# Kernel tuning notes

Measured on AMD Instinct MI355X. Metric: run time of the kernel, lower is better.

The kernel has to match this reference:

```python
import jax, jax.numpy as jnp
import numpy as np

N_FEATURES = 256
TOPK = 32
WINDOW = 128
EMBED = 128
BATCH = 64
ALPHA = 0.2  # LeakyReLU negative slope


def setup_inputs() -> dict:
    key = jax.random.key(0)
    ks = jax.random.split(key, 8)
    x_n = jax.random.normal(ks[0], (BATCH, N_FEATURES, WINDOW), jnp.float32)
    x_e = jax.random.normal(ks[1], (N_FEATURES, TOPK), jnp.float32)
    edge_indices = jax.random.randint(ks[2], (2, N_FEATURES * TOPK), 0, N_FEATURES, dtype=jnp.int32)
    all_embeddings = jax.random.normal(ks[3], (N_FEATURES, EMBED), jnp.float32)
    # lin_n: Linear(window_size, embed_dim)
    W_n = jax.random.normal(ks[4], (WINDOW, EMBED), jnp.float32) * (1.0 / np.sqrt(WINDOW))
    b_n = jax.random.normal(ks[5], (EMBED,), jnp.float32) * 0.01
    # attention vector a: [2*embed_dim, 1], xavier-like scale
    a = jax.random.normal(ks[6], (2 * EMBED, 1), jnp.float32) * (1.414 / np.sqrt(2 * EMBED))
    bias_n = jax.random.normal(ks[7], (N_FEATURES, TOPK), jnp.float32) * 0.02
    return {"x_n": x_n, "x_e": x_e, "edge_indices": edge_indices,
            "all_embeddings": all_embeddings, "W_n": W_n, "b_n": b_n,
            "a": a, "bias_n": bias_n}


def reference(x_n, x_e, edge_indices, all_embeddings, W_n, b_n, a, bias_n):
    B, NF, _ = x_n.shape
    K, E = TOPK, EMBED
    lrelu = lambda t: jax.nn.leaky_relu(t, negative_slope=ALPHA)

    # Wx_n = lin_n(x_n): [B, NF, E]
    Wx_n = jnp.einsum('bnw,we->bne', x_n, W_n) + b_n

    nbr = edge_indices[0].reshape(NF, K)  # neighbor ids per node

    # _make_node_attention_input (faithful, including the cat-then-view mixing):
    # repeat_interleave(K, dim=1) -> [B, NF, K, E]
    rep = jnp.broadcast_to(Wx_n[:, :, None, :], (B, NF, K, E))
    alt = Wx_n[:, nbr]  # gather: [B, NF, K, E]
    # cat on dim=2 -> [B, NF, 2K, E]; view -> [B, NF, K, 2E]
    a_input_n = jnp.concatenate([rep, alt], axis=2).reshape(B, NF, K, 2 * E)

    # e_n = leakyrelu(a_input_n @ a).squeeze(3): [B, NF, K]
    e_n = lrelu(jnp.einsum('bnkd,d->bnk', a_input_n, a[:, 0]))
    e_n = e_n + jnp.nan_to_num(bias_n)

    # softmax over topk neighbors; dropout is a no-op in eval mode
    attention_n = jax.nn.softmax(e_n, axis=2)

    # weighted aggregate of gathered neighbor features
    h_n = lrelu(attention_n[..., None] * alt)  # [B, NF, K, E]
    return h_n
```

## Files before the change

kernel.cpp:

```cpp
#include <hip/hip_runtime.h>

#define NFEAT 256
#define TK    32
#define WIN   128
#define EMB   128
#define NBATCH 64
#define ALPHA 0.2f
#define MROWS (NBATCH * NFEAT)

__device__ __forceinline__ float lrelu(float x) { return x > 0.f ? x : ALPHA * x; }

__global__ __launch_bounds__(256) void gemm_wx(
    const float* __restrict__ x,
    const float* __restrict__ W,
    const float* __restrict__ bn,
    const float* __restrict__ avec,
    float* __restrict__ wx,
    float* __restrict__ s1, float* __restrict__ s2) {
  __shared__ float xT[WIN][36];
  int t = threadIdx.x;
  int rows0 = blockIdx.x * 32;

  {
    int r = t >> 3, jc = t & 7;
    const float4* src = (const float4*)(x + (long)(rows0 + r) * WIN + jc * 16);
#pragma unroll
    for (int u = 0; u < 4; ++u) {
      float4 v = src[u];
      int c = jc * 16 + u * 4;
      xT[c + 0][r] = v.x; xT[c + 1][r] = v.y; xT[c + 2][r] = v.z; xT[c + 3][r] = v.w;
    }
  }
  __syncthreads();

  int g = t >> 5, ct = t & 31;
  int r0 = g * 4;
  int c0 = ct * 4;

  float acc[4][4];
#pragma unroll
  for (int i = 0; i < 4; ++i)
#pragma unroll
    for (int j = 0; j < 4; ++j) acc[i][j] = 0.f;

#pragma unroll 4
  for (int k = 0; k < WIN; ++k) {
    float4 xv = *(const float4*)&xT[k][r0];
    float4 wv = *(const float4*)(W + k * EMB + c0);
    acc[0][0] += xv.x * wv.x; acc[0][1] += xv.x * wv.y; acc[0][2] += xv.x * wv.z; acc[0][3] += xv.x * wv.w;
    acc[1][0] += xv.y * wv.x; acc[1][1] += xv.y * wv.y; acc[1][2] += xv.y * wv.z; acc[1][3] += xv.y * wv.w;
    acc[2][0] += xv.z * wv.x; acc[2][1] += xv.z * wv.y; acc[2][2] += xv.z * wv.z; acc[2][3] += xv.z * wv.w;
    acc[3][0] += xv.w * wv.x; acc[3][1] += xv.w * wv.y; acc[3][2] += xv.w * wv.z; acc[3][3] += xv.w * wv.w;
  }

  float4 bv = *(const float4*)(bn + c0);
#pragma unroll
  for (int i = 0; i < 4; ++i) {
    acc[i][0] += bv.x; acc[i][1] += bv.y; acc[i][2] += bv.z; acc[i][3] += bv.w;
  }

#pragma unroll
  for (int i = 0; i < 4; ++i) {
    float4 o = make_float4(acc[i][0], acc[i][1], acc[i][2], acc[i][3]);
    *(float4*)(wx + (long)(rows0 + r0 + i) * EMB + c0) = o;
  }

  float4 a1 = *(const float4*)(avec + c0);
  float4 a2 = *(const float4*)(avec + EMB + c0);
  float p1[4], p2[4];
#pragma unroll
  for (int i = 0; i < 4; ++i) {
    p1[i] = acc[i][0] * a1.x + acc[i][1] * a1.y + acc[i][2] * a1.z + acc[i][3] * a1.w;
    p2[i] = acc[i][0] * a2.x + acc[i][1] * a2.y + acc[i][2] * a2.z + acc[i][3] * a2.w;
  }
#pragma unroll
  for (int i = 0; i < 4; ++i) {
#pragma unroll
    for (int m = 1; m < 32; m <<= 1) {
      p1[i] += __shfl_xor(p1[i], m, 64);
      p2[i] += __shfl_xor(p2[i], m, 64);
    }
  }
  if (ct == 0) {
#pragma unroll
    for (int i = 0; i < 4; ++i) {
      s1[rows0 + r0 + i] = p1[i];
      s2[rows0 + r0 + i] = p2[i];
    }
  }
}

__global__ __launch_bounds__(256) void attn_out(
    const int* __restrict__ edge,
    const float* __restrict__ biasn,
    const float* __restrict__ wx,
    const float* __restrict__ s1, const float* __restrict__ s2,
    float* __restrict__ out) {
  __shared__ float att[TK];
  __shared__ int nbrS[TK];
  int bidx = blockIdx.x;
  int b = bidx >> 8, n = bidx & 255;
  int tid = threadIdx.x;

  if (tid < TK) {
    int k = tid;
    nbrS[k] = edge[n * TK + k];
    float v;
    if (k < 16) {
      v = s1[b * NFEAT + n] + s2[b * NFEAT + n];
    } else {
      int j0 = 2 * k - 32;
      int r0 = edge[n * TK + j0];
      int r1 = edge[n * TK + j0 + 1];
      v = s1[b * NFEAT + r0] + s2[b * NFEAT + r1];
    }
    v = lrelu(v);
    float bb = biasn[n * TK + k];
    if (bb != bb) bb = 0.f;
    v += bb;
    float mx = v;
#pragma unroll
    for (int m = 1; m < 32; m <<= 1) mx = fmaxf(mx, __shfl_xor(mx, m, 64));
    float ex = __expf(v - mx);
    float sum = ex;
#pragma unroll
    for (int m = 1; m < 32; m <<= 1) sum += __shfl_xor(sum, m, 64);
    att[k] = ex / sum;
  }
  __syncthreads();

#pragma unroll
  for (int p = 0; p < 2; ++p) {
    int k = (tid >> 4) + p * 16;
    int c0 = (tid & 15) * 8;
    long row = (long)b * NFEAT + nbrS[k];
    float ak = att[k];
    const float4* src = (const float4*)(wx + row * EMB + c0);
    float4 v0 = src[0], v1 = src[1];
    float4 o0 = make_float4(lrelu(ak * v0.x), lrelu(ak * v0.y), lrelu(ak * v0.z), lrelu(ak * v0.w));
    float4 o1 = make_float4(lrelu(ak * v1.x), lrelu(ak * v1.y), lrelu(ak * v1.z), lrelu(ak * v1.w));
    float4* dst = (float4*)(out + ((long)bidx * TK + k) * EMB + c0);
    dst[0] = o0; dst[1] = o1;
  }
}

extern "C" void kernel_launch(void* const* d_in, const int* in_sizes, int n_in,
                              void* d_out, int out_size, void* d_ws, size_t ws_size,
                              hipStream_t stream) {
  const float* x_n    = (const float*)d_in[0];
  const int*   edge   = (const int*)d_in[2];
  const float* W_n    = (const float*)d_in[4];
  const float* b_n    = (const float*)d_in[5];
  const float* a_v    = (const float*)d_in[6];
  const float* bias_n = (const float*)d_in[7];
  float* out = (float*)d_out;

  char* ws = (char*)d_ws;
  float* wx = (float*)ws;
  float* s1 = (float*)(ws + (8 << 20));
  float* s2 = (float*)(ws + (8 << 20) + (64 << 10));

  gemm_wx<<<MROWS / 32, 256, 0, stream>>>(x_n, W_n, b_n, a_v, wx, s1, s2);
  attn_out<<<NBATCH * NFEAT, 256, 0, stream>>>(edge, bias_n, wx, s1, s2, out);
}
```

Before: 312.2 us.

## Process eight nodes per block in attn_out and use nontemporal output stores

Each attn_out block now handles eight nodes instead of one. All 256 threads compute softmax attention weights for the eight nodes in parallel rather than only 32 threads, and the block then loops over the eight nodes to write the gathered, scaled output. Output writes use nontemporal stores so the large write-once result does not pollute cache. This cuts the block count eightfold and the idle-thread softmax phase, at the cost of fewer blocks for latency hiding.

```diff
diff --git a/kernel.cpp b/kernel.cpp
--- a/kernel.cpp
+++ b/kernel.cpp
@@ -7,6 +7,8 @@
 #define NBATCH 64
 #define ALPHA 0.2f
 #define MROWS (NBATCH * NFEAT)
+
+typedef float f32x4 __attribute__((ext_vector_type(4)));
 
 __device__ __forceinline__ float lrelu(float x) { return x > 0.f ? x : ALPHA * x; }
 
@@ -96,51 +98,62 @@
     const float* __restrict__ wx,
     const float* __restrict__ s1, const float* __restrict__ s2,
     float* __restrict__ out) {
-  __shared__ float att[TK];
-  __shared__ int nbrS[TK];
+  __shared__ float att[8][TK];
+  __shared__ int nbrS[8][TK];
   int bidx = blockIdx.x;
-  int b = bidx >> 8, n = bidx & 255;
+  int b  = bidx >> 5;
+  int n0 = (bidx & 31) << 3;
   int tid = threadIdx.x;
+  int k  = tid & 31;
+  int nl = tid >> 5;
+  int n  = n0 + nl;
 
-  if (tid < TK) {
-    int k = tid;
-    nbrS[k] = edge[n * TK + k];
-    float v;
-    if (k < 16) {
-      v = s1[b * NFEAT + n] + s2[b * NFEAT + n];
-    } else {
-      int j0 = 2 * k - 32;
-      int r0 = edge[n * TK + j0];
-      int r1 = edge[n * TK + j0 + 1];
-      v = s1[b * NFEAT + r0] + s2[b * NFEAT + r1];
-    }
-    v = lrelu(v);
-    float bb = biasn[n * TK + k];
-    if (bb != bb) bb = 0.f;
-    v += bb;
-    float mx = v;
+  nbrS[nl][k] = edge[n * TK + k];
+  float v;
+  if (k < 16) {
+    v = s1[b * NFEAT + n] + s2[b * NFEAT + n];
+  } else {
+    int j0 = 2 * k - 32;
+    int r0 = edge[n * TK + j0];
+    int r1 = edge[n * TK + j0 + 1];
+    v = s1[b * NFEAT + r0] + s2[b * NFEAT + r1];
+  }
+  v = lrelu(v);
+  float bb = biasn[n * TK + k];
+  if (bb != bb) bb = 0.f;
+  v += bb;
+  float mx = v;
 #pragma unroll
-    for (int m = 1; m < 32; m <<= 1) mx = fmaxf(mx, __shfl_xor(mx, m, 64));
-    float ex = __expf(v - mx);
-    float sum = ex;
+  for (int m = 1; m < 32; m <<= 1) mx = fmaxf(mx, __shfl_xor(mx, m, 64));
+  float ex = __expf(v - mx);
+  float sum = ex;
 #pragma unroll
-    for (int m = 1; m < 32; m <<= 1) sum += __shfl_xor(sum, m, 64);
-    att[k] = ex / sum;
-  }
+  for (int m = 1; m < 32; m <<= 1) sum += __shfl_xor(sum, m, 64);
+  att[nl][k] = ex / sum;
   __syncthreads();
 
+  int kk = tid >> 4;
+  int c0 = (tid & 15) * 8;
+  const long wrow_base = (long)b * NFEAT;
+  float* oblk = out + ((long)(b * NFEAT + n0)) * TK * EMB;
+#pragma unroll 2
+  for (int nn = 0; nn < 8; ++nn) {
 #pragma unroll
-  for (int p = 0; p < 2; ++p) {
-    int k = (tid >> 4) + p * 16;
-    int c0 = (tid & 15) * 8;
-    long row = (long)b * NFEAT + nbrS[k];
-    float ak = att[k];
-    const float4* src = (const float4*)(wx + row * EMB + c0);
-    float4 v0 = src[0], v1 = src[1];
-    float4 o0 = make_float4(lrelu(ak * v0.x), lrelu(ak * v0.y), lrelu(ak * v0.z), lrelu(ak * v0.w));
-    float4 o1 = make_float4(lrelu(ak * v1.x), lrelu(ak * v1.y), lrelu(ak * v1.z), lrelu(ak * v1.w));
-    float4* dst = (float4*)(out + ((long)bidx * TK + k) * EMB + c0);
-    dst[0] = o0; dst[1] = o1;
+    for (int p = 0; p < 2; ++p) {
+      int k2 = kk + p * 16;
+      float ak = att[nn][k2];
+      long row = wrow_base + nbrS[nn][k2];
+      const f32x4* src = (const f32x4*)(wx + row * EMB + c0);
+      f32x4 v0 = src[0], v1 = src[1];
+      f32x4 o0, o1;
+      o0.x = lrelu(ak * v0.x); o0.y = lrelu(ak * v0.y);
+      o0.z = lrelu(ak * v0.z); o0.w = lrelu(ak * v0.w);
+      o1.x = lrelu(ak * v1.x); o1.y = lrelu(ak * v1.y);
+      o1.z = lrelu(ak * v1.z); o1.w = lrelu(ak * v1.w);
+      f32x4* dst = (f32x4*)(oblk + ((long)nn * TK + k2) * EMB + c0);
+      __builtin_nontemporal_store(o0, dst);
+      __builtin_nontemporal_store(o1, dst + 1);
+    }
   }
 }
 
@@ -161,5 +174,5 @@
   float* s2 = (float*)(ws + (8 << 20) + (64 << 10));
 
   gemm_wx<<<MROWS / 32, 256, 0, stream>>>(x_n, W_n, b_n, a_v, wx, s1, s2);
-  attn_out<<<NBATCH * NFEAT, 256, 0, stream>>>(edge, bias_n, wx, s1, s2, out);
+  attn_out<<<NBATCH * NFEAT / 8, 256, 0, stream>>>(edge, bias_n, wx, s1, s2, out);
 }
```

Result: slower. 363.3 us (+16.4%).
